# Kernel tuning notes

Hardware: AMD Instinct MI355X
Metric: run time of the kernel (lower is better)

## Reference

```python
import jax, jax.numpy as jnp
import numpy as np

D = 256      # d_model
H = 8        # n_heads
HD = D // H  # head_dim = 32
P = 16       # point dim per head


def setup_inputs() -> dict:
    key = jax.random.key(0)
    ks = jax.random.split(key, 12)
    B, S = 2, 2048
    w = lambda k, shape: jax.random.normal(k, shape, jnp.float32) * 0.02
    return {
        "seq_repr": jax.random.normal(ks[0], (B, S, D), jnp.float32),
        "coords": jax.random.normal(ks[1], (B, S, 3, 3), jnp.float32),
        "frames": jax.random.normal(ks[2], (B, S, 4), jnp.float32),
        "mask": jnp.ones((B, S), jnp.int32),
        "Wq": w(ks[3], (D, D)), "bq": jnp.zeros((D,), jnp.float32),
        "Wk": w(ks[4], (D, D)), "bk": jnp.zeros((D,), jnp.float32),
        "Wv": w(ks[5], (D, D)), "bv": jnp.zeros((D,), jnp.float32),
        "Wpq": w(ks[6], (3, H * P)), "bpq": jnp.zeros((H * P,), jnp.float32),
        "Wpk": w(ks[7], (3, H * P)), "bpk": jnp.zeros((H * P,), jnp.float32),
        "Wo": w(ks[8], (D, D)), "bo": jnp.zeros((D,), jnp.float32),
        "Wpo": w(ks[9], (H * P, 3)), "bpo": jnp.zeros((3,), jnp.float32),
        "attn_bias": jnp.zeros((H,), jnp.float32),
    }


def reference(seq_repr, coords, frames, mask, Wq, bq, Wk, bk, Wv, bv,
              Wpq, bpq, Wpk, bpk, Wo, bo, Wpo, bpo, attn_bias):
    B, S, _ = seq_repr.shape
    q = (seq_repr @ Wq + bq).reshape(B, S, H, HD)
    k = (seq_repr @ Wk + bk).reshape(B, S, H, HD)
    v = (seq_repr @ Wv + bv).reshape(B, S, H, HD)

    rep = coords[..., 1, :]                                  # [B,S,3] representative atom
    pq = (rep @ Wpq + bpq).reshape(B, S, H, P)
    pk = (rep @ Wpk + bpk).reshape(B, S, H, P)

    scale = 1.0 / np.sqrt(HD)
    scores = (jnp.einsum('bihd,bjhd->bhij', q, k) * scale
              + jnp.einsum('bihp,bjhp->bhij', pq, pk) * 0.25  # 1/sqrt(16)
              + attn_bias[None, :, None, None])

    mask2d = (mask[:, :, None] * mask[:, None, :])[:, None]  # [B,1,S,S]
    scores = jnp.where(mask2d == 0, jnp.float32(-1e9), scores)

    w = jax.nn.softmax(scores, axis=-1)                      # [B,H,S,S]

    seq_ctx = jnp.einsum('bhij,bjhd->bihd', w, v).reshape(B, S, D)
    pt_ctx = jnp.einsum('bhij,bjhp->bihp', w, pq).reshape(B, S, H * P)

    seq_out = seq_ctx @ Wo + bo                              # [B,S,D]
    point_out = pt_ctx @ Wpo + bpo                           # [B,S,3]
    return (seq_out, point_out)
```

## Files before the change

kernel.cpp:

```cpp
#include <hip/hip_runtime.h>
#include <hip/hip_bf16.h>

#define D_ 256
#define H_ 8
#define B_ 2
#define S_ 2048
#define MTOT 4096
#define AUGQ 64
#define NBH 16
#define KPAD 72
#define NSPLIT 2
#define NJ 16
#define LOG2E 1.4426950408889634f

typedef __attribute__((ext_vector_type(8))) short short8;
typedef __attribute__((ext_vector_type(4))) short short4v;
typedef __attribute__((ext_vector_type(4))) float f32x4;

static __device__ __forceinline__ short bf16_of(float f) {
  union { __hip_bfloat16 h; short s; } u;
  u.h = __float2bfloat16(f);
  return u.s;
}
static __device__ __forceinline__ float f_of_bf16(short s) {
  union { float f; unsigned int u; } u;
  u.u = ((unsigned int)(unsigned short)s) << 16;
  return u.f;
}

static __device__ __forceinline__ f32x4 mfma16(short4v a, short4v b, f32x4 c) {
#if defined(__has_builtin) && __has_builtin(__builtin_amdgcn_mfma_f32_16x16x16bf16_1k)
  return __builtin_amdgcn_mfma_f32_16x16x16bf16_1k(a, b, c, 0, 0, 0);
#else
  asm("v_mfma_f32_16x16x16_bf16 %0, %1, %2, %0" : "+v"(c) : "v"(a), "v"(b));
  return c;
#endif
}


__global__ void prep_all(const float* __restrict__ Wq, const float* __restrict__ Wk,
                         const float* __restrict__ Wv, const float* __restrict__ Wo,
                         const float* __restrict__ coords, const int* __restrict__ mask,
                         const float* __restrict__ Wpq, const float* __restrict__ bpq,
                         const float* __restrict__ Wpk, const float* __restrict__ bpk,
                         short* __restrict__ Wqkv_t, short* __restrict__ Wo_t,
                         short* __restrict__ Qa, short* __restrict__ Ka,
                         short* __restrict__ VaT) {
  int gid = blockIdx.x * 256 + threadIdx.x;
  int NT = gridDim.x * 256;
  for (int idx = gid; idx < 768 * 256; idx += NT) {
    int n = idx >> 8, k = idx & 255;
    const float* W = (n < 256) ? Wq : (n < 512 ? Wk : Wv);
    Wqkv_t[idx] = bf16_of(W[k * 256 + (n & 255)]);
  }
  for (int idx = gid; idx < 256 * 256; idx += NT) {
    int n = idx >> 8, k = idx & 255;
    Wo_t[idx] = bf16_of(Wo[k * 256 + n]);
  }
  for (int idx = gid; idx < MTOT * 8; idx += NT) {
    int m = idx >> 3, h = idx & 7;
    int b = m >> 11, s = m & 2047;
    float r0 = coords[m * 9 + 3], r1 = coords[m * 9 + 4], r2 = coords[m * 9 + 5];
    size_t base = ((size_t)(b * 8 + h) * S_ + s) * AUGQ;
    short8 pqv[2], pkv[2];
#pragma unroll
    for (int c = 0; c < 2; c++)
#pragma unroll
      for (int i = 0; i < 8; i++) {
        int j = h * 16 + c * 8 + i;
        float pq = r0 * Wpq[j] + r1 * Wpq[128 + j] + r2 * Wpq[256 + j] + bpq[j];
        float pk = r0 * Wpk[j] + r1 * Wpk[128 + j] + r2 * Wpk[256 + j] + bpk[j];
        pqv[c][i] = bf16_of(pq * LOG2E);
        pkv[c][i] = bf16_of(pk * 0.25f);
      }
    short8 padq = {};
    padq[0] = bf16_of(LOG2E);
    short8 padk = {};
    padk[0] = mask[m] ? (short)0 : bf16_of(-1e9f);
    short8 z = {};
    *reinterpret_cast<short8*>(&Qa[base + 32]) = pqv[0];
    *reinterpret_cast<short8*>(&Qa[base + 40]) = pqv[1];
    *reinterpret_cast<short8*>(&Qa[base + 48]) = padq;
    *reinterpret_cast<short8*>(&Qa[base + 56]) = z;
    *reinterpret_cast<short8*>(&Ka[base + 32]) = pkv[0];
    *reinterpret_cast<short8*>(&Ka[base + 40]) = pkv[1];
    *reinterpret_cast<short8*>(&Ka[base + 48]) = padk;
    *reinterpret_cast<short8*>(&Ka[base + 56]) = z;
  }
  for (int idx = gid; idx < NBH * 16 * (S_ / 8); idx += NT) {
    int s8 = idx & 255, p = (idx >> 8) & 15, bh = idx >> 12;
    int b = bh >> 3, h = bh & 7, j = h * 16 + p;
    float w0 = Wpq[j], w1 = Wpq[128 + j], w2 = Wpq[256 + j], bb = bpq[j];
    short8 o;
#pragma unroll
    for (int i = 0; i < 8; i++) {
      int m = b * 2048 + s8 * 8 + i;
      o[i] = bf16_of(coords[m * 9 + 3] * w0 + coords[m * 9 + 4] * w1 +
                     coords[m * 9 + 5] * w2 + bb);
    }
    *reinterpret_cast<short8*>(&VaT[((size_t)bh * 48 + 32 + p) * S_ + s8 * 8]) = o;
  }
}


__global__ __launch_bounds__(256) void qkv_gemm(
    const float* __restrict__ X, const short* __restrict__ Wt,
    const float* __restrict__ bq, const float* __restrict__ bk, const float* __restrict__ bv,
    short* __restrict__ Qa, short* __restrict__ Ka, short* __restrict__ VaT) {
  __shared__ __align__(16) short As[64 * 136];
  __shared__ __align__(16) short Bs[64 * 136];
  int m0 = blockIdx.x * 64, n0 = blockIdx.y * 64;
  int tid = threadIdx.x, lane = tid & 63, w = tid >> 6;
  int t = lane & 15, g = lane >> 4, kf = g * 8;
  int wr = (w >> 1) * 32, wc = (w & 1) * 32;
  f32x4 acc[2][2] = {};
  int srow = tid >> 2, skc = (tid & 3) * 32;
  for (int ph = 0; ph < 2; ph++) {
    int k0 = ph * 128;
    __syncthreads();
    {
      const float* xs = &X[(size_t)(m0 + srow) * 256 + k0 + skc];
      short4v av[8];
#pragma unroll
      for (int i = 0; i < 8; i++) {
        f32x4 xv = *reinterpret_cast<const f32x4*>(&xs[i * 4]);
        short4v o;
        o[0] = bf16_of(xv[0]); o[1] = bf16_of(xv[1]);
        o[2] = bf16_of(xv[2]); o[3] = bf16_of(xv[3]);
        av[i] = o;
      }
#pragma unroll
      for (int i = 0; i < 8; i++)
        *reinterpret_cast<short4v*>(&As[srow * 136 + skc + i * 4]) = av[i];
      const uint4* wsrc = reinterpret_cast<const uint4*>(&Wt[(size_t)(n0 + srow) * 256 + k0 + skc]);
#pragma unroll
      for (int i = 0; i < 4; i++)
        *reinterpret_cast<uint4*>(&Bs[srow * 136 + skc + i * 8]) = wsrc[i];
    }
    __syncthreads();
#pragma unroll
    for (int kk = 0; kk < 4; kk++) {
      short8 a[2], bb[2];
#pragma unroll
      for (int i = 0; i < 2; i++)
        a[i] = *reinterpret_cast<const short8*>(&As[(wr + i * 16 + t) * 136 + kk * 32 + kf]);
#pragma unroll
      for (int jj = 0; jj < 2; jj++)
        bb[jj] = *reinterpret_cast<const short8*>(&Bs[(wc + jj * 16 + t) * 136 + kk * 32 + kf]);
#pragma unroll
      for (int i = 0; i < 2; i++)
#pragma unroll
        for (int jj = 0; jj < 2; jj++)
          acc[i][jj] = __builtin_amdgcn_mfma_f32_16x16x32_bf16(a[i], bb[jj], acc[i][jj], 0, 0, 0);
    }
  }
  __syncthreads();
  short* Cs = As;
  const float scale = 0.17677669529663687f * LOG2E;
  int b = m0 >> 11, sbase = m0 & 2047;
#pragma unroll
  for (int i = 0; i < 2; i++)
#pragma unroll
    for (int jj = 0; jj < 2; jj++)
#pragma unroll
      for (int r = 0; r < 4; r++) {
        int rl = wr + i * 16 + g * 4 + r;
        int cl = wc + jj * 16 + t;
        int n = n0 + cl;
        float v = acc[i][jj][r];
        if (n < 256) v = (v + bq[n]) * scale;
        else if (n < 512) v = v + bk[n - 256];
        else v = v + bv[n - 512];
        Cs[rl * 72 + cl] = bf16_of(v);
      }
  __syncthreads();
  if (n0 < 512) {
#pragma unroll
    for (int i2 = 0; i2 < 2; i2++) {
      int task = tid + i2 * 256;
      int row = task >> 3, c = task & 7;
      int n = n0 + c * 8;
      short* dst = (n < 256) ? Qa : Ka;
      int nn = n & 255;
      int hh = nn >> 5, d = nn & 31;
      *reinterpret_cast<short8*>(&dst[((size_t)(b * 8 + hh) * S_ + sbase + row) * AUGQ + d]) =
          *reinterpret_cast<const short8*>(&Cs[row * 72 + c * 8]);
    }
  } else {
    int hv0 = (n0 - 512) >> 5;
#pragma unroll
    for (int i2 = 0; i2 < 2; i2++) {
      int task = tid + i2 * 256;
      int fl = task >> 3, s8 = task & 7;
      short8 o;
#pragma unroll
      for (int i = 0; i < 8; i++) o[i] = Cs[(s8 * 8 + i) * 72 + fl];
      int hh = hv0 + (fl >> 5), d = fl & 31;
      *reinterpret_cast<short8*>(&VaT[((size_t)(b * 8 + hh) * 48 + d) * S_ + sbase + s8 * 8]) = o;
    }
  }
}


__global__ __launch_bounds__(256, 2) void attn(
    const short* __restrict__ Qa, const short* __restrict__ Ka,
    const short* __restrict__ VaT,
    short* __restrict__ Ctx, float* __restrict__ AccL) {
  __shared__ __align__(16) char smem[32256];

  int bid = blockIdx.x;
  int xcd = bid & 7, slot = bid >> 3;
  int gidx = xcd * 4 + (slot >> 4);
  int it = slot & 15;
  int split = gidx & 1;
  int bhv = gidx >> 1;

  int tid = threadIdx.x, lane = tid & 63, w = tid >> 6;
  int t = lane & 15, g = lane >> 4, kf = g * 8;
  int q0w = it * 128 + w * 32;
  size_t bh = (size_t)bhv * S_;

  short8 aq[2][2];
#pragma unroll
  for (int g2 = 0; g2 < 2; g2++)
#pragma unroll
    for (int c = 0; c < 2; c++)
      aq[g2][c] = *reinterpret_cast<const short8*>(
          &Qa[(bh + q0w + g2 * 16 + t) * AUGQ + c * 32 + kf]);

  f32x4 OaccA[3] = {}, OaccB[3] = {};
  float lsum0 = 0.f, lsum1 = 0.f;

  uint4 kreg0, kreg1, vreg0, vreg1;
  int srow = tid >> 3, sko = (tid & 7) * 8;
  const int jt0 = split * NJ;

  auto issue = [&](int jt) {
    const uint4* ks = reinterpret_cast<const uint4*>(&Ka[(bh + jt * 64) * AUGQ]);
    kreg0 = ks[tid];
    kreg1 = ks[tid + 256];
    size_t vb = (size_t)bhv * 48 * S_ + jt * 64;
    vreg0 = *reinterpret_cast<const uint4*>(&VaT[vb + (size_t)srow * S_ + sko]);
    if (tid < 128)
      vreg1 = *reinterpret_cast<const uint4*>(&VaT[vb + (size_t)(srow + 32) * S_ + sko]);
  };
  auto commit = [&](int buf) {
    short* Kd = (short*)(smem + buf * 9216);
    short* Vd = (short*)(smem + 18432 + buf * 6912);
    *reinterpret_cast<uint4*>(&Kd[srow * KPAD + sko]) = kreg0;
    *reinterpret_cast<uint4*>(&Kd[(srow + 32) * KPAD + sko]) = kreg1;
    *reinterpret_cast<uint4*>(&Vd[srow * KPAD + sko]) = vreg0;
    if (tid < 128)
      *reinterpret_cast<uint4*>(&Vd[(srow + 32) * KPAD + sko]) = vreg1;
  };

  issue(jt0);
  commit(0);
  __syncthreads();

  for (int j = 0; j < NJ; j++) {
    int cur = j & 1;
    if (j + 1 < NJ) issue(jt0 + j + 1);
    const short* Kc = (const short*)(smem + cur * 9216);
    const short* Vc = (const short*)(smem + 18432 + cur * 6912);
    short4v pbA[4], pbB[4];
#pragma unroll
    for (int sub = 0; sub < 4; sub++) {
      short8 ka0 = *reinterpret_cast<const short8*>(&Kc[(sub * 16 + t) * KPAD + kf]);
      short8 ka1 = *reinterpret_cast<const short8*>(&Kc[(sub * 16 + t) * KPAD + 32 + kf]);
      f32x4 sA = {}, sB = {};
      sA = __builtin_amdgcn_mfma_f32_16x16x32_bf16(ka0, aq[0][0], sA, 0, 0, 0);
      sA = __builtin_amdgcn_mfma_f32_16x16x32_bf16(ka1, aq[0][1], sA, 0, 0, 0);
      sB = __builtin_amdgcn_mfma_f32_16x16x32_bf16(ka0, aq[1][0], sB, 0, 0, 0);
      sB = __builtin_amdgcn_mfma_f32_16x16x32_bf16(ka1, aq[1][1], sB, 0, 0, 0);
      float a0 = exp2f(sA[0]), a1 = exp2f(sA[1]), a2 = exp2f(sA[2]), a3 = exp2f(sA[3]);
      float b0 = exp2f(sB[0]), b1 = exp2f(sB[1]), b2 = exp2f(sB[2]), b3 = exp2f(sB[3]);
      lsum0 += (a0 + a1) + (a2 + a3);
      lsum1 += (b0 + b1) + (b2 + b3);
      short4v pa, pb;
      pa[0] = bf16_of(a0); pa[1] = bf16_of(a1); pa[2] = bf16_of(a2); pa[3] = bf16_of(a3);
      pb[0] = bf16_of(b0); pb[1] = bf16_of(b1); pb[2] = bf16_of(b2); pb[3] = bf16_of(b3);
      pbA[sub] = pa; pbB[sub] = pb;
    }
    __builtin_amdgcn_s_setprio(1);
#pragma unroll
    for (int tt = 0; tt < 3; tt++) {
#pragma unroll
      for (int sub = 0; sub < 4; sub++) {
        short4v va = *reinterpret_cast<const short4v*>(&Vc[(tt * 16 + t) * KPAD + sub * 16 + g * 4]);
        OaccA[tt] = mfma16(va, pbA[sub], OaccA[tt]);
        OaccB[tt] = mfma16(va, pbB[sub], OaccB[tt]);
      }
    }
    __builtin_amdgcn_s_setprio(0);
    if (j + 1 < NJ) commit(cur ^ 1);
    __syncthreads();
  }

  lsum0 += __shfl_xor(lsum0, 16); lsum0 += __shfl_xor(lsum0, 32);
  lsum1 += __shfl_xor(lsum1, 16); lsum1 += __shfl_xor(lsum1, 32);

  float* Of = (float*)smem;
#pragma unroll
  for (int tt = 0; tt < 3; tt++)
#pragma unroll
    for (int r = 0; r < 4; r++) {
      Of[(w * 32 + t) * 52 + tt * 16 + g * 4 + r] = OaccA[tt][r];
      Of[(w * 32 + 16 + t) * 52 + tt * 16 + g * 4 + r] = OaccB[tt][r];
    }
  if (lane < 16) {
    size_t lb = (size_t)(split * NBH + bhv) * S_ + q0w + lane;
    AccL[lb] = lsum0;
    AccL[lb + 16] = lsum1;
  }
  __syncthreads();
  short* CtxP = Ctx + (size_t)split * NBH * S_ * 48;
  size_t obase = bh + it * 128;
  for (int task = tid; task < 768; task += 256) {
    int row = task / 6, c8 = task % 6;
    const float* src = &Of[row * 52 + c8 * 8];
    short8 o;
#pragma unroll
    for (int i = 0; i < 8; i++) o[i] = bf16_of(src[i]);
    *reinterpret_cast<short8*>(&CtxP[(obase + row) * 48 + c8 * 8]) = o;
  }
}


__global__ __launch_bounds__(512) void out_gemm(
    const short* __restrict__ Ctx, const float* __restrict__ AccL,
    const short* __restrict__ Wot, const float* __restrict__ bo,
    const float* __restrict__ Wpo, const float* __restrict__ bpo,
    float* __restrict__ Out) {
  const size_t CTXSZ = (size_t)NBH * S_ * 48;
  int m0 = blockIdx.x * 64;
  int tid = threadIdx.x;
  int b = m0 >> 11, sbase = m0 & 2047;

  if (blockIdx.y == 4) {
    int row = tid >> 3, hh = tid & 7;
    int m = m0 + row, s = sbase + row;
    size_t rowO = (size_t)(b * 8 + hh) * S_ + s;
    float inv = 1.0f / (AccL[rowO] + AccL[(size_t)NBH * S_ + rowO]);
    float a0 = 0.f, a1 = 0.f, a2 = 0.f;
#pragma unroll
    for (int half = 0; half < 2; half++) {
      short8 v0 = *reinterpret_cast<const short8*>(&Ctx[rowO * 48 + 32 + half * 8]);
      short8 v1 = *reinterpret_cast<const short8*>(&Ctx[CTXSZ + rowO * 48 + 32 + half * 8]);
#pragma unroll
      for (int c = 0; c < 8; c++) {
        float val = (f_of_bf16(v0[c]) + f_of_bf16(v1[c])) * inv;
        int j = hh * 16 + half * 8 + c;
        a0 += val * Wpo[j * 3 + 0];
        a1 += val * Wpo[j * 3 + 1];
        a2 += val * Wpo[j * 3 + 2];
      }
    }
    a0 += __shfl_xor(a0, 1); a0 += __shfl_xor(a0, 2); a0 += __shfl_xor(a0, 4);
    a1 += __shfl_xor(a1, 1); a1 += __shfl_xor(a1, 2); a1 += __shfl_xor(a1, 4);
    a2 += __shfl_xor(a2, 1); a2 += __shfl_xor(a2, 2); a2 += __shfl_xor(a2, 4);
    if (hh == 0) {
      float* po = Out + (size_t)MTOT * 256;
      po[(size_t)m * 3 + 0] = a0 + bpo[0];
      po[(size_t)m * 3 + 1] = a1 + bpo[1];
      po[(size_t)m * 3 + 2] = a2 + bpo[2];
    }
    return;
  }

  __shared__ __align__(16) short As[64 * 136];
  __shared__ __align__(16) short Bs[64 * 136];
  int n0 = blockIdx.y * 64;
  int lane = tid & 63, w = tid >> 6;
  int t = lane & 15, g = lane >> 4, kf = g * 8;
  int wm = w & 3, wn = w >> 2;
  f32x4 acc[2] = {};
  int srow = tid >> 3, skc = (tid & 7) * 16;
  for (int ph = 0; ph < 2; ph++) {
    int k0 = ph * 128;
    __syncthreads();
    {
      int kg = k0 + skc;
      int hh = kg >> 5, d0 = kg & 31;
      size_t rowO = (size_t)(b * 8 + hh) * S_ + sbase + srow;
      float inv = 1.0f / (AccL[rowO] + AccL[(size_t)NBH * S_ + rowO]);
#pragma unroll
      for (int half = 0; half < 2; half++) {
        short8 a0 = *reinterpret_cast<const short8*>(&Ctx[rowO * 48 + d0 + half * 8]);
        short8 a1 = *reinterpret_cast<const short8*>(&Ctx[CTXSZ + rowO * 48 + d0 + half * 8]);
        short8 o;
#pragma unroll
        for (int c = 0; c < 8; c++)
          o[c] = bf16_of((f_of_bf16(a0[c]) + f_of_bf16(a1[c])) * inv);
        *reinterpret_cast<short8*>(&As[srow * 136 + skc + half * 8]) = o;
      }
      *reinterpret_cast<uint4*>(&Bs[srow * 136 + skc]) =
          *reinterpret_cast<const uint4*>(&Wot[(size_t)(n0 + srow) * 256 + kg]);
      *reinterpret_cast<uint4*>(&Bs[srow * 136 + skc + 8]) =
          *reinterpret_cast<const uint4*>(&Wot[(size_t)(n0 + srow) * 256 + kg + 8]);
    }
    __syncthreads();
#pragma unroll
    for (int kk = 0; kk < 4; kk++) {
      short8 a = *reinterpret_cast<const short8*>(&As[(wm * 16 + t) * 136 + kk * 32 + kf]);
#pragma unroll
      for (int jj = 0; jj < 2; jj++) {
        short8 bb = *reinterpret_cast<const short8*>(&Bs[(wn * 32 + jj * 16 + t) * 136 + kk * 32 + kf]);
        acc[jj] = __builtin_amdgcn_mfma_f32_16x16x32_bf16(a, bb, acc[jj], 0, 0, 0);
      }
    }
  }
#pragma unroll
  for (int jj = 0; jj < 2; jj++)
#pragma unroll
    for (int r = 0; r < 4; r++) {
      int mrow = m0 + wm * 16 + g * 4 + r;
      int n = n0 + wn * 32 + jj * 16 + t;
      Out[(size_t)mrow * 256 + n] = acc[jj][r] + bo[n];
    }
}


extern "C" void kernel_launch(void* const* d_in, const int* in_sizes, int n_in,
                              void* d_out, int out_size, void* d_ws, size_t ws_size,
                              hipStream_t stream) {
  const float* seq    = (const float*)d_in[0];
  const float* coords = (const float*)d_in[1];
  const int*   mask   = (const int*)d_in[3];
  const float* Wq  = (const float*)d_in[4];
  const float* bq  = (const float*)d_in[5];
  const float* Wk  = (const float*)d_in[6];
  const float* bk  = (const float*)d_in[7];
  const float* Wv  = (const float*)d_in[8];
  const float* bv  = (const float*)d_in[9];
  const float* Wpq = (const float*)d_in[10];
  const float* bpq = (const float*)d_in[11];
  const float* Wpk = (const float*)d_in[12];
  const float* bpk = (const float*)d_in[13];
  const float* Wo  = (const float*)d_in[14];
  const float* bo  = (const float*)d_in[15];
  const float* Wpo = (const float*)d_in[16];
  const float* bpo = (const float*)d_in[17];
  float* out = (float*)d_out;

  char* ws = (char*)d_ws;
  short* Wqkv_t = (short*)ws; ws += 768 * 256 * 2;
  short* Wo_t   = (short*)ws; ws += 256 * 256 * 2;
  short* Qa     = (short*)ws; ws += (size_t)NBH * S_ * AUGQ * 2;
  short* Ka     = (short*)ws; ws += (size_t)NBH * S_ * AUGQ * 2;
  short* VaT    = (short*)ws; ws += (size_t)NBH * 48 * S_ * 2;
  short* Ctx    = (short*)ws; ws += (size_t)NSPLIT * NBH * S_ * 48 * 2;
  float* AccL   = (float*)ws; ws += (size_t)NSPLIT * NBH * S_ * 4;

  prep_all<<<1024, 256, 0, stream>>>(Wq, Wk, Wv, Wo, coords, mask, Wpq, bpq, Wpk, bpk,
                                     Wqkv_t, Wo_t, Qa, Ka, VaT);
  qkv_gemm<<<dim3(64, 12), 256, 0, stream>>>(seq, Wqkv_t, bq, bk, bv, Qa, Ka, VaT);
  attn<<<512, 256, 0, stream>>>(Qa, Ka, VaT, Ctx, AccL);
  out_gemm<<<dim3(64, 5), 512, 0, stream>>>(Ctx, AccL, Wo_t, bo, Wpo, bpo, out);
}
```

Before: 69.52 us.

## Split attention keys four ways and use 16x16x32 MFMA for PV with permuted V layout

Doubles the key-dimension split of the attention kernel from two to four, launching twice as many blocks with a higher occupancy hint, and sums four partial contexts and normalizers in the output GEMM. Separately, the P·V product moves from 16x16x16 to 16x16x32 bf16 MFMA by packing probabilities into 8-wide vectors. The V transpose gains a within-64 sequence permutation so columns line up with the score register layout. This aims for more parallelism and fewer MFMA issues, but adds partial-buffer traffic and reduction work in the epilogue, and the workspace for Ctx/AccL must grow.

```diff
diff --git a/kernel.cpp b/kernel.cpp
--- a/kernel.cpp
+++ b/kernel.cpp
@@ -9,8 +9,8 @@
 #define AUGQ 64
 #define NBH 16
 #define KPAD 72
-#define NSPLIT 2
-#define NJ 16
+#define NSPLIT 4
+#define NJ 8
 #define LOG2E 1.4426950408889634f
 
 typedef __attribute__((ext_vector_type(8))) short short8;
@@ -28,13 +28,8 @@
   return u.f;
 }
 
-static __device__ __forceinline__ f32x4 mfma16(short4v a, short4v b, f32x4 c) {
-#if defined(__has_builtin) && __has_builtin(__builtin_amdgcn_mfma_f32_16x16x16bf16_1k)
-  return __builtin_amdgcn_mfma_f32_16x16x16bf16_1k(a, b, c, 0, 0, 0);
-#else
-  asm("v_mfma_f32_16x16x16_bf16 %0, %1, %2, %0" : "+v"(c) : "v"(a), "v"(b));
-  return c;
-#endif
+static __device__ __forceinline__ int sinv64(int c) {
+  return (((((c >> 2) & 1) << 1) | ((c >> 5) & 1)) << 4) + (((c >> 3) & 3) << 2) + (c & 3);
 }
 
 
@@ -94,7 +89,8 @@
     short8 o;
 #pragma unroll
     for (int i = 0; i < 8; i++) {
-      int m = b * 2048 + s8 * 8 + i;
+      int c = (s8 & 7) * 8 + i;
+      int m = b * 2048 + (s8 >> 3) * 64 + sinv64(c);
       o[i] = bf16_of(coords[m * 9 + 3] * w0 + coords[m * 9 + 4] * w1 +
                      coords[m * 9 + 5] * w2 + bb);
     }
@@ -194,7 +190,7 @@
       int fl = task >> 3, s8 = task & 7;
       short8 o;
 #pragma unroll
-      for (int i = 0; i < 8; i++) o[i] = Cs[(s8 * 8 + i) * 72 + fl];
+      for (int i = 0; i < 8; i++) o[i] = Cs[sinv64(s8 * 8 + i) * 72 + fl];
       int hh = hv0 + (fl >> 5), d = fl & 31;
       *reinterpret_cast<short8*>(&VaT[((size_t)(b * 8 + hh) * 48 + d) * S_ + sbase + s8 * 8]) = o;
     }
@@ -202,7 +198,7 @@
 }
 
 
-__global__ __launch_bounds__(256, 2) void attn(
+__global__ __launch_bounds__(256, 4) void attn(
     const short* __restrict__ Qa, const short* __restrict__ Ka,
     const short* __restrict__ VaT,
     short* __restrict__ Ctx, float* __restrict__ AccL) {
@@ -210,10 +206,10 @@
 
   int bid = blockIdx.x;
   int xcd = bid & 7, slot = bid >> 3;
-  int gidx = xcd * 4 + (slot >> 4);
+  int gidx = xcd * 8 + (slot >> 4);
   int it = slot & 15;
-  int split = gidx & 1;
-  int bhv = gidx >> 1;
+  int split = gidx & 3;
+  int bhv = gidx >> 2;
 
   int tid = threadIdx.x, lane = tid & 63, w = tid >> 6;
   int t = lane & 15, g = lane >> 4, kf = g * 8;
@@ -263,7 +259,7 @@
     if (j + 1 < NJ) issue(jt0 + j + 1);
     const short* Kc = (const short*)(smem + cur * 9216);
     const short* Vc = (const short*)(smem + 18432 + cur * 6912);
-    short4v pbA[4], pbB[4];
+    short8 pA[2], pB[2];
 #pragma unroll
     for (int sub = 0; sub < 4; sub++) {
       short8 ka0 = *reinterpret_cast<const short8*>(&Kc[(sub * 16 + t) * KPAD + kf]);
@@ -277,19 +273,20 @@
       float b0 = exp2f(sB[0]), b1 = exp2f(sB[1]), b2 = exp2f(sB[2]), b3 = exp2f(sB[3]);
       lsum0 += (a0 + a1) + (a2 + a3);
       lsum1 += (b0 + b1) + (b2 + b3);
-      short4v pa, pb;
-      pa[0] = bf16_of(a0); pa[1] = bf16_of(a1); pa[2] = bf16_of(a2); pa[3] = bf16_of(a3);
-      pb[0] = bf16_of(b0); pb[1] = bf16_of(b1); pb[2] = bf16_of(b2); pb[3] = bf16_of(b3);
-      pbA[sub] = pa; pbB[sub] = pb;
+      int ww = sub & 1, off = (sub >> 1) * 4;
+      pA[ww][off + 0] = bf16_of(a0); pA[ww][off + 1] = bf16_of(a1);
+      pA[ww][off + 2] = bf16_of(a2); pA[ww][off + 3] = bf16_of(a3);
+      pB[ww][off + 0] = bf16_of(b0); pB[ww][off + 1] = bf16_of(b1);
+      pB[ww][off + 2] = bf16_of(b2); pB[ww][off + 3] = bf16_of(b3);
     }
     __builtin_amdgcn_s_setprio(1);
 #pragma unroll
     for (int tt = 0; tt < 3; tt++) {
 #pragma unroll
-      for (int sub = 0; sub < 4; sub++) {
-        short4v va = *reinterpret_cast<const short4v*>(&Vc[(tt * 16 + t) * KPAD + sub * 16 + g * 4]);
-        OaccA[tt] = mfma16(va, pbA[sub], OaccA[tt]);
-        OaccB[tt] = mfma16(va, pbB[sub], OaccB[tt]);
+      for (int w2 = 0; w2 < 2; w2++) {
+        short8 va = *reinterpret_cast<const short8*>(&Vc[(tt * 16 + t) * KPAD + w2 * 32 + kf]);
+        OaccA[tt] = __builtin_amdgcn_mfma_f32_16x16x32_bf16(va, pA[w2], OaccA[tt], 0, 0, 0);
+        OaccB[tt] = __builtin_amdgcn_mfma_f32_16x16x32_bf16(va, pB[w2], OaccB[tt], 0, 0, 0);
       }
     }
     __builtin_amdgcn_s_setprio(0);
@@ -341,15 +338,23 @@
     int row = tid >> 3, hh = tid & 7;
     int m = m0 + row, s = sbase + row;
     size_t rowO = (size_t)(b * 8 + hh) * S_ + s;
-    float inv = 1.0f / (AccL[rowO] + AccL[(size_t)NBH * S_ + rowO]);
+    float l = 0.f;
+#pragma unroll
+    for (int sp = 0; sp < NSPLIT; sp++) l += AccL[(size_t)sp * NBH * S_ + rowO];
+    float inv = 1.0f / l;
     float a0 = 0.f, a1 = 0.f, a2 = 0.f;
 #pragma unroll
     for (int half = 0; half < 2; half++) {
-      short8 v0 = *reinterpret_cast<const short8*>(&Ctx[rowO * 48 + 32 + half * 8]);
-      short8 v1 = *reinterpret_cast<const short8*>(&Ctx[CTXSZ + rowO * 48 + 32 + half * 8]);
+      float sum[8] = {};
+#pragma unroll
+      for (int sp = 0; sp < NSPLIT; sp++) {
+        short8 v = *reinterpret_cast<const short8*>(&Ctx[sp * CTXSZ + rowO * 48 + 32 + half * 8]);
+#pragma unroll
+        for (int c = 0; c < 8; c++) sum[c] += f_of_bf16(v[c]);
+      }
 #pragma unroll
       for (int c = 0; c < 8; c++) {
-        float val = (f_of_bf16(v0[c]) + f_of_bf16(v1[c])) * inv;
+        float val = sum[c] * inv;
         int j = hh * 16 + half * 8 + c;
         a0 += val * Wpo[j * 3 + 0];
         a1 += val * Wpo[j * 3 + 1];
@@ -383,15 +388,22 @@
       int kg = k0 + skc;
       int hh = kg >> 5, d0 = kg & 31;
       size_t rowO = (size_t)(b * 8 + hh) * S_ + sbase + srow;
-      float inv = 1.0f / (AccL[rowO] + AccL[(size_t)NBH * S_ + rowO]);
+      float l = 0.f;
+#pragma unroll
+      for (int sp = 0; sp < NSPLIT; sp++) l += AccL[(size_t)sp * NBH * S_ + rowO];
+      float inv = 1.0f / l;
 #pragma unroll
       for (int half = 0; half < 2; half++) {
-        short8 a0 = *reinterpret_cast<const short8*>(&Ctx[rowO * 48 + d0 + half * 8]);
-        short8 a1 = *reinterpret_cast<const short8*>(&Ctx[CTXSZ + rowO * 48 + d0 + half * 8]);
+        float sum[8] = {};
+#pragma unroll
+        for (int sp = 0; sp < NSPLIT; sp++) {
+          short8 a = *reinterpret_cast<const short8*>(&Ctx[sp * CTXSZ + rowO * 48 + d0 + half * 8]);
+#pragma unroll
+          for (int c = 0; c < 8; c++) sum[c] += f_of_bf16(a[c]);
+        }
         short8 o;
 #pragma unroll
-        for (int c = 0; c < 8; c++)
-          o[c] = bf16_of((f_of_bf16(a0[c]) + f_of_bf16(a1[c])) * inv);
+        for (int c = 0; c < 8; c++) o[c] = bf16_of(sum[c] * inv);
         *reinterpret_cast<short8*>(&As[srow * 136 + skc + half * 8]) = o;
       }
       *reinterpret_cast<uint4*>(&Bs[srow * 136 + skc]) =
@@ -455,6 +467,6 @@
   prep_all<<<1024, 256, 0, stream>>>(Wq, Wk, Wv, Wo, coords, mask, Wpq, bpq, Wpk, bpk,
                                      Wqkv_t, Wo_t, Qa, Ka, VaT);
   qkv_gemm<<<dim3(64, 12), 256, 0, stream>>>(seq, Wqkv_t, bq, bk, bv, Qa, Ka, VaT);
-  attn<<<512, 256, 0, stream>>>(Qa, Ka, VaT, Ctx, AccL);
+  attn<<<1024, 256, 0, stream>>>(Qa, Ka, VaT, Ctx, AccL);
   out_gemm<<<dim3(64, 5), 512, 0, stream>>>(Ctx, AccL, Wo_t, bo, Wpo, bpo, out);
 }
```

Result: faster. 65.76 us (-5.4%).
